# Performance work log

Hardware: AMD Instinct MI355X
Metric: run time of the kernel (lower is better)

The kernel has to match this reference:

```python
import jax, jax.numpy as jnp
import numpy as np
import math

B, N, C, S, H, E = 2, 20000, 512, 128, 8, 320000
D = C // H
EPS = 1e-6


def setup_inputs() -> dict:
    key = jax.random.key(0)
    ks = jax.random.split(key, 14)
    x = jax.random.normal(ks[0], (B, N, C), jnp.float32)
    adj_indices = jax.random.randint(ks[1], (2, E), 0, N)
    adj_values = jax.random.uniform(ks[2], (E,), jnp.float32)

    def lin(k, fi, fo):
        # stored as (in, out) so y = x @ W + b (equivalent to torch Linear)
        return jax.random.normal(k, (fi, fo), jnp.float32) / np.sqrt(fi).astype(np.float32)

    Ws = lin(ks[3], C, S); bs = jnp.zeros((S,), jnp.float32)
    Wq = lin(ks[4], C, C); bq = jnp.zeros((C,), jnp.float32)
    Wk = lin(ks[5], C, C); bk = jnp.zeros((C,), jnp.float32)
    Wv = lin(ks[6], C, C); bv = jnp.zeros((C,), jnp.float32)
    Wo = lin(ks[7], C, C); bo = jnp.zeros((C,), jnp.float32)
    beta_raw = jnp.float32(math.log(math.expm1(0.13)))
    return {"x": x, "adj_indices": adj_indices, "adj_values": adj_values,
            "Ws": Ws, "bs": bs, "Wq": Wq, "bq": bq, "Wk": Wk, "bk": bk,
            "Wv": Wv, "bv": bv, "Wo": Wo, "bo": bo, "beta_raw": beta_raw}


def reference(x, adj_indices, adj_values, Ws, bs, Wq, bq, Wk, bk, Wv, bv, Wo, bo, beta_raw):
    # slice assignment weights: (B, N, S)
    weights = jax.nn.softmax(x @ Ws + bs, axis=-1)
    # weight_sum -> (B, S, 1), clamped
    wsum = jnp.maximum(weights.sum(axis=1), EPS)[:, :, None]
    slices = jnp.einsum('bns,bnc->bsc', weights, x) / wsum  # (B, S, C)

    # sparse adjacency aggregation: y[b, r] = sum_e v_e * weights[b, col_e]
    rows, cols = adj_indices[0], adj_indices[1]
    msg = jnp.take(weights, cols, axis=1) * adj_values[None, :, None]  # (B, E, S)
    graph_weights = jax.vmap(lambda m: jax.ops.segment_sum(m, rows, num_segments=N))(msg)  # (B, N, S)

    gb = jnp.einsum('bns,bnt->bst', weights, graph_weights)  # (B, S, S)
    gb = 0.5 * (gb + jnp.swapaxes(gb, 1, 2))
    gb = gb / jnp.maximum(gb.sum(axis=-1, keepdims=True), EPS)
    gb = jnp.log(jnp.maximum(gb, EPS))

    def heads(t, W, b):
        return (t @ W + b).reshape(B, S, H, D).transpose(0, 2, 1, 3)  # (B, H, S, D)

    q = heads(slices, Wq, bq)
    k = heads(slices, Wk, bk)
    v = heads(slices, Wv, bv)
    logits = jnp.einsum('bhqd,bhkd->bhqk', q, k) / math.sqrt(D)
    logits = logits + jax.nn.softplus(beta_raw) * gb[:, None]
    attn = jax.nn.softmax(logits, axis=-1)
    slices_out = jnp.einsum('bhqk,bhkd->bhqd', attn, v).transpose(0, 2, 1, 3).reshape(B, S, C)
    slices_out = slices_out @ Wo + bo
    return jnp.einsum('bns,bsc->bnc', weights, slices_out)  # (B, N, C)
```

## Files before the change

kernel.cpp:

```cpp
#include <hip/hip_runtime.h>
#include <math.h>

#define Bn 2
#define Nn 20000
#define Cn 512
#define Sn 128
#define Hn 8
#define Dn 64
#define En 320000
#define EPSf 1e-6f
#define NB64 313
#define NB128 157

#define S_CHUNK 320
#define S_KB 63
#define G_CHUNK 128
#define G_KB 157

typedef __attribute__((ext_vector_type(4))) float f32x4;
typedef __attribute__((ext_vector_type(8))) short s16x8;

__device__ __forceinline__ unsigned short f2bf(float f) {
    unsigned u = __float_as_uint(f);
    return (unsigned short)((u + 0x7fffu + ((u >> 16) & 1u)) >> 16);
}
__device__ __forceinline__ float bf2f(unsigned short h) {
    return __uint_as_float(((unsigned)h) << 16);
}

__device__ __forceinline__ unsigned lds_off(int row, int n) {
    unsigned ch = ((((unsigned)n >> 3) ^ ((unsigned)row & 7u) ^ (((unsigned)row >> 3) & 7u)) & 7u);
    return (unsigned)row * 128u + ch * 16u + ((unsigned)n & 7u) * 2u;
}

__device__ __forceinline__ void stage_bf16tile(
    const unsigned short* __restrict__ src, int stride, int nvalid, unsigned* dst, int t)
{
    #pragma unroll
    for (int l = 0; l < 2; l++) {
        int task = t + l * 256;
        int row = task >> 2, seg = task & 3;
        s16x8 a = {0,0,0,0,0,0,0,0}, b = {0,0,0,0,0,0,0,0};
        if (row < nvalid) {
            a = *(const s16x8*)(src + (size_t)row * stride + seg * 16);
            b = *(const s16x8*)(src + (size_t)row * stride + seg * 16 + 8);
        }
        *(s16x8*)((char*)dst + lds_off(row, seg * 16)) = a;
        *(s16x8*)((char*)dst + lds_off(row, seg * 16 + 8)) = b;
    }
}

__device__ __forceinline__ void stage_pairtile(
    const unsigned short* __restrict__ src, int stride, int c0,
    int nbase, int nlimit, unsigned* dst, int t)
{
    int c = t & 15;
    int p0 = t >> 4;
    #pragma unroll
    for (int half = 0; half < 2; half++) {
        int pp = p0 + half * 16;
        int nl = 2 * pp;
        int ng = nbase + nl;
        s16x8 a0 = {0,0,0,0,0,0,0,0}, a1 = {0,0,0,0,0,0,0,0};
        if (ng < nlimit)     a0 = *(const s16x8*)(src + (size_t)ng * stride + c0 + 8 * c);
        if (ng + 1 < nlimit) a1 = *(const s16x8*)(src + (size_t)(ng + 1) * stride + c0 + 8 * c);
        #pragma unroll
        for (int i = 0; i < 8; i++) {
            unsigned val = ((unsigned)(unsigned short)a0[i]) |
                           (((unsigned)(unsigned short)a1[i]) << 16);
            dst[lds_off(8 * c + i, nl) >> 2] = val;
        }
    }
}

__device__ __forceinline__ void stage_tilesF(
    const unsigned short* __restrict__ wA, const float* __restrict__ Bsrc,
    int Bstride, int c0, int nbase, unsigned* At32, unsigned* Bt32, int t)
{
    int c = t & 15;
    int p0 = t >> 4;
    #pragma unroll
    for (int half = 0; half < 2; half++) {
        int pp = p0 + half * 16;
        int nl = 2 * pp;
        int ng = nbase + nl;
        s16x8 a0 = {0,0,0,0,0,0,0,0}, a1 = {0,0,0,0,0,0,0,0};
        if (ng < Nn)     a0 = *(const s16x8*)(wA + (size_t)ng * Sn + 8 * c);
        if (ng + 1 < Nn) a1 = *(const s16x8*)(wA + (size_t)(ng + 1) * Sn + 8 * c);
        #pragma unroll
        for (int i = 0; i < 8; i++) {
            unsigned val = ((unsigned)(unsigned short)a0[i]) |
                           (((unsigned)(unsigned short)a1[i]) << 16);
            At32[lds_off(8 * c + i, nl) >> 2] = val;
        }
        float b0[8], b1[8];
        if (ng < Nn) {
            float4 v0 = *(const float4*)(Bsrc + (size_t)ng * Bstride + c0 + 8 * c);
            float4 v1 = *(const float4*)(Bsrc + (size_t)ng * Bstride + c0 + 8 * c + 4);
            b0[0]=v0.x; b0[1]=v0.y; b0[2]=v0.z; b0[3]=v0.w;
            b0[4]=v1.x; b0[5]=v1.y; b0[6]=v1.z; b0[7]=v1.w;
        } else {
            #pragma unroll
            for (int i = 0; i < 8; i++) b0[i] = 0.f;
        }
        if (ng + 1 < Nn) {
            float4 v0 = *(const float4*)(Bsrc + (size_t)(ng + 1) * Bstride + c0 + 8 * c);
            float4 v1 = *(const float4*)(Bsrc + (size_t)(ng + 1) * Bstride + c0 + 8 * c + 4);
            b1[0]=v0.x; b1[1]=v0.y; b1[2]=v0.z; b1[3]=v0.w;
            b1[4]=v1.x; b1[5]=v1.y; b1[6]=v1.z; b1[7]=v1.w;
        } else {
            #pragma unroll
            for (int i = 0; i < 8; i++) b1[i] = 0.f;
        }
        #pragma unroll
        for (int i = 0; i < 8; i++) {
            unsigned val = (unsigned)f2bf(b0[i]) | (((unsigned)f2bf(b1[i])) << 16);
            Bt32[lds_off(8 * c + i, nl) >> 2] = val;
        }
    }
}

__global__ __launch_bounds__(256) void k_prepWsT(
    const float* __restrict__ Ws, unsigned short* __restrict__ WsT)
{
    __shared__ float tile[32][33];
    int t = threadIdx.x;
    int k0 = blockIdx.x * 32;
    int s0 = blockIdx.y * 32;
    #pragma unroll
    for (int l = 0; l < 4; l++) {
        int idx = t + l * 256;
        int r = idx >> 5, c = idx & 31;
        tile[r][c] = Ws[(size_t)(k0 + r) * Sn + s0 + c];
    }
    __syncthreads();
    #pragma unroll
    for (int l = 0; l < 4; l++) {
        int idx = t + l * 256;
        int r = idx >> 5, c = idx & 31;
        WsT[(size_t)(s0 + r) * Cn + k0 + c] = f2bf(tile[c][r]);
    }
}

__global__ __launch_bounds__(256) void k_prepWT(
    const float* __restrict__ Wq, const float* __restrict__ Wk,
    const float* __restrict__ Wv, const float* __restrict__ Wo,
    unsigned short* __restrict__ WT)
{
    __shared__ float tile[32][33];
    int t = threadIdx.x;
    int z = blockIdx.z;
    const float* W = (z == 0) ? Wq : (z == 1) ? Wk : (z == 2) ? Wv : Wo;
    unsigned short* dst = WT + (size_t)z * Cn * Cn;
    int k0 = blockIdx.x * 32;
    int c0 = blockIdx.y * 32;
    #pragma unroll
    for (int l = 0; l < 4; l++) {
        int idx = t + l * 256;
        int r = idx >> 5, c = idx & 31;
        tile[r][c] = W[(size_t)(k0 + r) * Cn + c0 + c];
    }
    __syncthreads();
    #pragma unroll
    for (int l = 0; l < 4; l++) {
        int idx = t + l * 256;
        int r = idx >> 5, c = idx & 31;
        dst[(size_t)(c0 + r) * Cn + k0 + c] = f2bf(tile[c][r]);
    }
}

__global__ __launch_bounds__(256) void k_assign2(
    const float* __restrict__ x, const unsigned short* __restrict__ WsT,
    const float* __restrict__ bs, unsigned short* __restrict__ weights,
    float* __restrict__ wsum)
{
    __shared__ __align__(16) unsigned At32[2048];
    __shared__ __align__(16) unsigned Bt32[4096];
    __shared__ float wsum_loc[128];

    int t = threadIdx.x;
    int lane = t & 63;
    int wid = t >> 6;
    int l15 = lane & 15, lg = lane >> 4;
    int blk = blockIdx.x;
    int b = blk / NB64;
    int rb = blk % NB64;
    int n0 = rb * 64;
    int nvalid = Nn - n0; if (nvalid > 64) nvalid = 64;
    const float* xb = x + (size_t)b * Nn * Cn;

    if (t < 128) wsum_loc[t] = 0.f;

    f32x4 acc[8];
    const f32x4 fz = {0.f, 0.f, 0.f, 0.f};
    #pragma unroll
    for (int j = 0; j < 8; j++) acc[j] = fz;

    for (int ks = 0; ks < 8; ks++) {
        {
            int row = t >> 2, seg = t & 3;
            float v[16];
            if (row < nvalid) {
                const float4* p = (const float4*)(xb + (size_t)(n0 + row) * Cn + ks * 64 + seg * 16);
                float4 a = p[0], bq = p[1], c = p[2], d = p[3];
                v[0]=a.x; v[1]=a.y; v[2]=a.z; v[3]=a.w;
                v[4]=bq.x; v[5]=bq.y; v[6]=bq.z; v[7]=bq.w;
                v[8]=c.x; v[9]=c.y; v[10]=c.z; v[11]=c.w;
                v[12]=d.x; v[13]=d.y; v[14]=d.z; v[15]=d.w;
            } else {
                #pragma unroll
                for (int i = 0; i < 16; i++) v[i] = 0.f;
            }
            #pragma unroll
            for (int h = 0; h < 2; h++) {
                uint4 u;
                u.x = (unsigned)f2bf(v[h*8+0]) | (((unsigned)f2bf(v[h*8+1])) << 16);
                u.y = (unsigned)f2bf(v[h*8+2]) | (((unsigned)f2bf(v[h*8+3])) << 16);
                u.z = (unsigned)f2bf(v[h*8+4]) | (((unsigned)f2bf(v[h*8+5])) << 16);
                u.w = (unsigned)f2bf(v[h*8+6]) | (((unsigned)f2bf(v[h*8+7])) << 16);
                *(uint4*)((char*)At32 + lds_off(row, seg * 16 + h * 8)) = u;
            }
        }
        stage_bf16tile(WsT + ks * 64, Cn, 128, Bt32, t);
        __syncthreads();
        #pragma unroll
        for (int m = 0; m < 2; m++) {
            s16x8 af = *(const s16x8*)((const char*)At32 +
                       lds_off(wid * 16 + l15, m * 32 + lg * 8));
            #pragma unroll
            for (int j = 0; j < 8; j++) {
                s16x8 bf = *(const s16x8*)((const char*)Bt32 +
                           lds_off(j * 16 + l15, m * 32 + lg * 8));
                acc[j] = __builtin_amdgcn_mfma_f32_16x16x32_bf16(af, bf, acc[j], 0, 0, 0);
            }
        }
        __syncthreads();
    }

    float bsv[8];
    #pragma unroll
    for (int j = 0; j < 8; j++) bsv[j] = bs[j * 16 + l15];

    unsigned short* wb = weights + (size_t)b * Nn * Sn;
    float wacc[8] = {0.f,0.f,0.f,0.f,0.f,0.f,0.f,0.f};
    #pragma unroll
    for (int r = 0; r < 4; r++) {
        float lv[8];
        #pragma unroll
        for (int j = 0; j < 8; j++) lv[j] = acc[j][r] + bsv[j];
        float m = lv[0];
        #pragma unroll
        for (int j = 1; j < 8; j++) m = fmaxf(m, lv[j]);
        m = fmaxf(m, __shfl_xor(m, 1));
        m = fmaxf(m, __shfl_xor(m, 2));
        m = fmaxf(m, __shfl_xor(m, 4));
        m = fmaxf(m, __shfl_xor(m, 8));
        float e[8], sm = 0.f;
        #pragma unroll
        for (int j = 0; j < 8; j++) { e[j] = __expf(lv[j] - m); sm += e[j]; }
        sm += __shfl_xor(sm, 1);
        sm += __shfl_xor(sm, 2);
        sm += __shfl_xor(sm, 4);
        sm += __shfl_xor(sm, 8);
        float inv = 1.f / sm;
        int n = n0 + wid * 16 + lg * 4 + r;
        bool valid = (n < Nn);
        #pragma unroll
        for (int j = 0; j < 8; j++) {
            float w = e[j] * inv;
            if (valid) {
                wb[(size_t)n * Sn + j * 16 + l15] = f2bf(w);
                wacc[j] += w;
            }
        }
    }
    #pragma unroll
    for (int j = 0; j < 8; j++) {
        wacc[j] += __shfl_xor(wacc[j], 16);
        wacc[j] += __shfl_xor(wacc[j], 32);
    }
    if (lg == 0) {
        #pragma unroll
        for (int j = 0; j < 8; j++) atomicAdd(&wsum_loc[j * 16 + l15], wacc[j]);
    }
    __syncthreads();
    if (t < 128) atomicAdd(&wsum[b * Sn + t], wsum_loc[t]);
}

__global__ __launch_bounds__(256) void k_deg(
    const int* __restrict__ adj, int* __restrict__ deg)
{
    int e = blockIdx.x * 256 + threadIdx.x;
    if (e < En) atomicAdd(&deg[adj[e]], 1);
}

__global__ __launch_bounds__(1024) void k_scan(
    const int* __restrict__ deg, int* __restrict__ offs)
{
    __shared__ int wsums[16];
    __shared__ int excl[16];
    __shared__ int runsS;
    __shared__ int totS;
    int t = threadIdx.x;
    int lane = t & 63;
    int w = t >> 6;
    if (t == 0) { offs[0] = 0; runsS = 0; }
    __syncthreads();
    for (int base = 0; base < Nn; base += 1024) {
        int v = (base + t < Nn) ? deg[base + t] : 0;
        int sv = v;
        #pragma unroll
        for (int d = 1; d < 64; d <<= 1) {
            int u = __shfl_up(sv, d);
            if (lane >= d) sv += u;
        }
        if (lane == 63) wsums[w] = sv;
        __syncthreads();
        if (t < 16) {
            int xv = wsums[t];
            int sw = xv;
            #pragma unroll
            for (int d = 1; d < 16; d <<= 1) {
                int u = __shfl_up(sw, d);
                if (t >= d) sw += u;
            }
            excl[t] = sw - xv;
            if (t == 15) totS = sw;
        }
        __syncthreads();
        if (base + t < Nn) offs[base + t + 1] = runsS + excl[w] + sv;
        __syncthreads();
        if (t == 0) runsS += totS;
        __syncthreads();
    }
}

__global__ __launch_bounds__(256) void k_fill(
    const int* __restrict__ adj, const float* __restrict__ vals,
    const int* __restrict__ offs, int* __restrict__ cursor,
    int2* __restrict__ epack)
{
    int e = blockIdx.x * 256 + threadIdx.x;
    if (e < En) {
        int r = adj[e];
        int p = atomicAdd(&cursor[r], 1);
        epack[offs[r] + p] = make_int2(adj[En + e], __float_as_int(vals[e]));
    }
}

__global__ __launch_bounds__(128) void k_gather(
    const unsigned short* __restrict__ weights, const int2* __restrict__ epack,
    const int* __restrict__ offs, unsigned short* __restrict__ gwb)
{
    int r = blockIdx.x;
    int s = threadIdx.x;
    int o0 = offs[r], o1 = offs[r + 1];
    const unsigned short* w0 = weights;
    const unsigned short* w1 = weights + (size_t)Nn * Sn;
    float a0 = 0.f, a1 = 0.f;
    int j = o0;
    for (; j + 4 <= o1; j += 4) {
        int2 e0 = epack[j], e1 = epack[j + 1], e2 = epack[j + 2], e3 = epack[j + 3];
        float v0 = __int_as_float(e0.y), v1 = __int_as_float(e1.y);
        float v2 = __int_as_float(e2.y), v3 = __int_as_float(e3.y);
        float p00 = bf2f(w0[(size_t)e0.x * Sn + s]);
        float p01 = bf2f(w1[(size_t)e0.x * Sn + s]);
        float p10 = bf2f(w0[(size_t)e1.x * Sn + s]);
        float p11 = bf2f(w1[(size_t)e1.x * Sn + s]);
        float p20 = bf2f(w0[(size_t)e2.x * Sn + s]);
        float p21 = bf2f(w1[(size_t)e2.x * Sn + s]);
        float p30 = bf2f(w0[(size_t)e3.x * Sn + s]);
        float p31 = bf2f(w1[(size_t)e3.x * Sn + s]);
        a0 += v0 * p00 + v1 * p10 + v2 * p20 + v3 * p30;
        a1 += v0 * p01 + v1 * p11 + v2 * p21 + v3 * p31;
    }
    for (; j < o1; j++) {
        int2 e = epack[j];
        float v = __int_as_float(e.y);
        a0 += v * bf2f(w0[(size_t)e.x * Sn + s]);
        a1 += v * bf2f(w1[(size_t)e.x * Sn + s]);
    }
    gwb[(size_t)r * Sn + s] = f2bf(a0);
    gwb[(size_t)Nn * Sn + (size_t)r * Sn + s] = f2bf(a1);
}

__global__ __launch_bounds__(256) void k_mmS(
    const unsigned short* __restrict__ wAall, const float* __restrict__ xall,
    float* __restrict__ partial)
{
    __shared__ __align__(16) unsigned At32[4096];
    __shared__ __align__(16) unsigned Bt32[4096];
    int t = threadIdx.x;
    int lane = t & 63;
    int wid = t >> 6;
    int ws = wid & 1, wc = wid >> 1;
    int blk = blockIdx.x;
    int b = blk / (4 * S_KB);
    int rem = blk % (4 * S_KB);
    int cb = rem / S_KB;
    int kb = rem % S_KB;
    int n0 = kb * S_CHUNK;
    int c0 = cb * 128;
    const unsigned short* wA = wAall + (size_t)b * Nn * Sn;
    const float* Bsrc = xall + (size_t)b * Nn * Cn;

    f32x4 acc[4][4];
    const f32x4 fz = {0.f, 0.f, 0.f, 0.f};
    #pragma unroll
    for (int i = 0; i < 4; i++) {
        #pragma unroll
        for (int j = 0; j < 4; j++) acc[i][j] = fz;
    }

    int l15 = lane & 15, lg = lane >> 4;

    for (int kt = 0; kt < S_CHUNK; kt += 64) {
        stage_tilesF(wA, Bsrc, Cn, c0, n0 + kt, At32, Bt32, t);
        __syncthreads();
        #pragma unroll
        for (int m = 0; m < 2; m++) {
            s16x8 af[4], bfr[4];
            #pragma unroll
            for (int i = 0; i < 4; i++) {
                int row = ws * 64 + i * 16 + l15;
                af[i] = *(const s16x8*)((const char*)At32 + lds_off(row, m * 32 + lg * 8));
            }
            #pragma unroll
            for (int j = 0; j < 4; j++) {
                int row = wc * 64 + j * 16 + l15;
                bfr[j] = *(const s16x8*)((const char*)Bt32 + lds_off(row, m * 32 + lg * 8));
            }
            #pragma unroll
            for (int i = 0; i < 4; i++) {
                #pragma unroll
                for (int j = 0; j < 4; j++)
                    acc[i][j] = __builtin_amdgcn_mfma_f32_16x16x32_bf16(
                        af[i], bfr[j], acc[i][j], 0, 0, 0);
            }
        }
        __syncthreads();
    }

    float* pp = partial + (size_t)blk * 16384;
    #pragma unroll
    for (int i = 0; i < 4; i++) {
        int srow = ws * 64 + i * 16 + lg * 4;
        #pragma unroll
        for (int j = 0; j < 4; j++) {
            int ccol = wc * 64 + j * 16 + l15;
            #pragma unroll
            for (int r = 0; r < 4; r++)
                pp[(size_t)(srow + r) * 128 + ccol] = acc[i][j][r];
        }
    }
}

__global__ __launch_bounds__(256) void k_mmG(
    const unsigned short* __restrict__ wAall, const unsigned short* __restrict__ gwall,
    float* __restrict__ partial)
{
    __shared__ __align__(16) unsigned At32[4096];
    __shared__ __align__(16) unsigned Bt32[4096];
    int t = threadIdx.x;
    int lane = t & 63;
    int wid = t >> 6;
    int ws = wid & 1, wc = wid >> 1;
    int blk = blockIdx.x;
    int b = blk / G_KB;
    int kb = blk % G_KB;
    int n0 = kb * G_CHUNK;
    const unsigned short* wA = wAall + (size_t)b * Nn * Sn;
    const unsigned short* Bsrc = gwall + (size_t)b * Nn * Sn;

    f32x4 acc[4][4];
    const f32x4 fz = {0.f, 0.f, 0.f, 0.f};
    #pragma unroll
    for (int i = 0; i < 4; i++) {
        #pragma unroll
        for (int j = 0; j < 4; j++) acc[i][j] = fz;
    }

    int l15 = lane & 15, lg = lane >> 4;

    for (int kt = 0; kt < G_CHUNK; kt += 64) {
        stage_pairtile(wA, Sn, 0, n0 + kt, Nn, At32, t);
        stage_pairtile(Bsrc, Sn, 0, n0 + kt, Nn, Bt32, t);
        __syncthreads();
        #pragma unroll
        for (int m = 0; m < 2; m++) {
            s16x8 af[4], bfr[4];
            #pragma unroll
            for (int i = 0; i < 4; i++) {
                int row = ws * 64 + i * 16 + l15;
                af[i] = *(const s16x8*)((const char*)At32 + lds_off(row, m * 32 + lg * 8));
            }
            #pragma unroll
            for (int j = 0; j < 4; j++) {
                int row = wc * 64 + j * 16 + l15;
                bfr[j] = *(const s16x8*)((const char*)Bt32 + lds_off(row, m * 32 + lg * 8));
            }
            #pragma unroll
            for (int i = 0; i < 4; i++) {
                #pragma unroll
                for (int j = 0; j < 4; j++)
                    acc[i][j] = __builtin_amdgcn_mfma_f32_16x16x32_bf16(
                        af[i], bfr[j], acc[i][j], 0, 0, 0);
            }
        }
        __syncthreads();
    }

    float* pp = partial + (size_t)blk * 16384;
    #pragma unroll
    for (int i = 0; i < 4; i++) {
        int srow = ws * 64 + i * 16 + lg * 4;
        #pragma unroll
        for (int j = 0; j < 4; j++) {
            int ccol = wc * 64 + j * 16 + l15;
            #pragma unroll
            for (int r = 0; r < 4; r++)
                pp[(size_t)(srow + r) * 128 + ccol] = acc[i][j][r];
        }
    }
}

__global__ __launch_bounds__(256) void k_reduceS(
    const float* __restrict__ partial, const float* __restrict__ wsum,
    unsigned short* __restrict__ sl16)
{
    int g = blockIdx.x * 256 + threadIdx.x;
    int c = g & 127;
    int s = (g >> 7) & 127;
    int cb = (g >> 14) & 3;
    int b = g >> 16;
    const float* pp = partial + (size_t)(b * 4 + cb) * S_KB * 16384 + (size_t)s * 128 + c;
    float sum = 0.f;
    #pragma unroll 7
    for (int kb = 0; kb < S_KB; kb++) sum += pp[(size_t)kb * 16384];
    sl16[((size_t)b * Sn + s) * Cn + cb * 128 + c] =
        f2bf(sum / fmaxf(wsum[b * Sn + s], EPSf));
}

__global__ __launch_bounds__(256) void k_reduceG(
    const float* __restrict__ partial, float* __restrict__ gb_raw)
{
    int g = blockIdx.x * 256 + threadIdx.x;
    int t2 = g & 127;
    int s = (g >> 7) & 127;
    int b = g >> 14;
    const float* pp = partial + (size_t)b * G_KB * 16384 + (size_t)s * 128 + t2;
    float sum = 0.f;
    #pragma unroll 8
    for (int kb = 0; kb < G_KB; kb++) sum += pp[(size_t)kb * 16384];
    gb_raw[(size_t)b * 16384 + (size_t)s * 128 + t2] = sum;
}

__global__ __launch_bounds__(128) void k_gb_fin(
    const float* __restrict__ gb_raw, float* __restrict__ gb)
{
    int bid = blockIdx.x;
    int b = bid >> 7, i = bid & 127;
    int j = threadIdx.x;
    const float* gr = gb_raw + (size_t)b * Sn * Sn;
    float sym = 0.5f * (gr[i * Sn + j] + gr[j * Sn + i]);
    float sum = sym;
    #pragma unroll
    for (int d = 1; d < 64; d <<= 1) sum += __shfl_xor(sum, d);
    __shared__ float wred[2];
    if ((j & 63) == 0) wred[j >> 6] = sum;
    __syncthreads();
    sum = wred[0] + wred[1];
    float r = fmaxf(sum, EPSf);
    gb[(size_t)b * Sn * Sn + (size_t)i * Sn + j] = logf(fmaxf(sym / r, EPSf));
}

__global__ __launch_bounds__(256) void k_qkv(
    const unsigned short* __restrict__ sl16, const unsigned short* __restrict__ WT,
    const float* __restrict__ bq, const float* __restrict__ bk,
    const float* __restrict__ bv,
    float* __restrict__ q, float* __restrict__ kb, float* __restrict__ vb)
{
    __shared__ __align__(16) unsigned At32[4096];
    __shared__ __align__(16) unsigned Bt32[4096];
    int t = threadIdx.x;
    int lane = t & 63;
    int wid = t >> 6;
    int ws = wid & 1, wc = wid >> 1;
    int l15 = lane & 15, lg = lane >> 4;
    int rb = blockIdx.x, cb = blockIdx.y, sel = blockIdx.z;
    const unsigned short* Bmat = WT + (size_t)sel * Cn * Cn;
    const float* bias = (sel == 0) ? bq : (sel == 1) ? bk : bv;
    float* outp = (sel == 0) ? q : (sel == 1) ? kb : vb;

    f32x4 acc[4][4];
    const f32x4 fz = {0.f, 0.f, 0.f, 0.f};
    #pragma unroll
    for (int i = 0; i < 4; i++) {
        #pragma unroll
        for (int j = 0; j < 4; j++) acc[i][j] = fz;
    }

    for (int ks = 0; ks < 8; ks++) {
        stage_bf16tile(sl16 + (size_t)rb * 128 * Cn + ks * 64, Cn, 128, At32, t);
        stage_bf16tile(Bmat + (size_t)cb * 128 * Cn + ks * 64, Cn, 128, Bt32, t);
        __syncthreads();
        #pragma unroll
        for (int m = 0; m < 2; m++) {
            s16x8 af[4], bfr[4];
            #pragma unroll
            for (int i = 0; i < 4; i++)
                af[i] = *(const s16x8*)((const char*)At32 +
                        lds_off(ws * 64 + i * 16 + l15, m * 32 + lg * 8));
            #pragma unroll
            for (int j = 0; j < 4; j++)
                bfr[j] = *(const s16x8*)((const char*)Bt32 +
                        lds_off(wc * 64 + j * 16 + l15, m * 32 + lg * 8));
            #pragma unroll
            for (int i = 0; i < 4; i++) {
                #pragma unroll
                for (int j = 0; j < 4; j++)
                    acc[i][j] = __builtin_amdgcn_mfma_f32_16x16x32_bf16(
                        af[i], bfr[j], acc[i][j], 0, 0, 0);
            }
        }
        __syncthreads();
    }

    float bvv[4];
    #pragma unroll
    for (int j = 0; j < 4; j++) bvv[j] = bias[cb * 128 + wc * 64 + j * 16 + l15];
    #pragma unroll
    for (int i = 0; i < 4; i++) {
        #pragma unroll
        for (int r = 0; r < 4; r++) {
            int m = rb * 128 + ws * 64 + i * 16 + lg * 4 + r;
            #pragma unroll
            for (int j = 0; j < 4; j++)
                outp[(size_t)m * Cn + cb * 128 + wc * 64 + j * 16 + l15] =
                    acc[i][j][r] + bvv[j];
        }
    }
}

__global__ __launch_bounds__(128) void k_attn(
    const float* __restrict__ q, const float* __restrict__ k,
    const float* __restrict__ v, const float* __restrict__ gb,
    const float* __restrict__ beta_raw, unsigned short* __restrict__ attn16)
{
    __shared__ float kv[128][65];
    __shared__ float qv[64];
    __shared__ float p[128];
    __shared__ float wred[2][2];

    int t = threadIdx.x;
    int bid = blockIdx.x;
    int b = bid / (Hn * Sn);
    int h = (bid / Sn) % Hn;
    int i = bid % Sn;
    size_t base = (size_t)b * Sn * Cn + (size_t)h * Dn;

    if (t < 64) qv[t] = q[base + (size_t)i * Cn + t];
    for (int l = 0; l < 64; l++) {
        int idx = t + l * 128;
        int j = idx >> 6, d = idx & 63;
        kv[j][d] = k[base + (size_t)j * Cn + d];
    }
    __syncthreads();

    float dot = 0.f;
    #pragma unroll
    for (int d = 0; d < 64; d++) dot += qv[d] * kv[t][d];

    float beta = log1pf(__expf(beta_raw[0]));
    float logit = dot * 0.125f + beta * gb[(size_t)b * Sn * Sn + (size_t)i * Sn + t];

    float m = logit;
    #pragma unroll
    for (int d = 1; d < 64; d <<= 1) m = fmaxf(m, __shfl_xor(m, d));
    if ((t & 63) == 0) wred[0][t >> 6] = m;
    __syncthreads();
    m = fmaxf(wred[0][0], wred[0][1]);
    float e = __expf(logit - m);
    float sm = e;
    #pragma unroll
    for (int d = 1; d < 64; d <<= 1) sm += __shfl_xor(sm, d);
    if ((t & 63) == 0) wred[1][t >> 6] = sm;
    __syncthreads();
    sm = wred[1][0] + wred[1][1];
    p[t] = e / sm;
    __syncthreads();

    for (int l = 0; l < 64; l++) {
        int idx = t + l * 128;
        int j = idx >> 6, d = idx & 63;
        kv[j][d] = v[base + (size_t)j * Cn + d];
    }
    __syncthreads();

    if (t < 64) {
        float o = 0.f;
        #pragma unroll 8
        for (int j = 0; j < 128; j++) o += p[j] * kv[j][t];
        attn16[base + (size_t)i * Cn + t] = f2bf(o);
    }
}

__global__ __launch_bounds__(256) void k_wo(
    const unsigned short* __restrict__ attn16, const unsigned short* __restrict__ WoT,
    const float* __restrict__ bo, unsigned short* __restrict__ SoT)
{
    __shared__ __align__(16) unsigned At32[4096];
    __shared__ __align__(16) unsigned Bt32[4096];
    int t = threadIdx.x;
    int lane = t & 63;
    int wid = t >> 6;
    int ws = wid & 1, wc = wid >> 1;
    int l15 = lane & 15, lg = lane >> 4;
    int b = blockIdx.x, cb = blockIdx.y;

    f32x4 acc[4][4];
    const f32x4 fz = {0.f, 0.f, 0.f, 0.f};
    #pragma unroll
    for (int i = 0; i < 4; i++) {
        #pragma unroll
        for (int j = 0; j < 4; j++) acc[i][j] = fz;
    }

    for (int ks = 0; ks < 8; ks++) {
        stage_bf16tile(attn16 + (size_t)b * 128 * Cn + ks * 64, Cn, 128, At32, t);
        stage_bf16tile(WoT + (size_t)cb * 128 * Cn + ks * 64, Cn, 128, Bt32, t);
        __syncthreads();
        #pragma unroll
        for (int m = 0; m < 2; m++) {
            s16x8 af[4], bfr[4];
            #pragma unroll
            for (int i = 0; i < 4; i++)
                af[i] = *(const s16x8*)((const char*)At32 +
                        lds_off(ws * 64 + i * 16 + l15, m * 32 + lg * 8));
            #pragma unroll
            for (int j = 0; j < 4; j++)
                bfr[j] = *(const s16x8*)((const char*)Bt32 +
                        lds_off(wc * 64 + j * 16 + l15, m * 32 + lg * 8));
            #pragma unroll
            for (int i = 0; i < 4; i++) {
                #pragma unroll
                for (int j = 0; j < 4; j++)
                    acc[i][j] = __builtin_amdgcn_mfma_f32_16x16x32_bf16(
                        af[i], bfr[j], acc[i][j], 0, 0, 0);
            }
        }
        __syncthreads();
    }

    float bvv[4];
    #pragma unroll
    for (int j = 0; j < 4; j++) bvv[j] = bo[cb * 128 + wc * 64 + j * 16 + l15];
    unsigned short* sb = SoT + (size_t)b * Cn * Sn;
    #pragma unroll
    for (int i = 0; i < 4; i++) {
        #pragma unroll
        for (int j = 0; j < 4; j++) {
            int c = cb * 128 + wc * 64 + j * 16 + l15;
            #pragma unroll
            for (int r = 0; r < 4; r++) {
                int s = ws * 64 + i * 16 + lg * 4 + r;
                sb[(size_t)c * Sn + s] = f2bf(acc[i][j][r] + bvv[j]);
            }
        }
    }
}

__global__ __launch_bounds__(256) void k_out2(
    const unsigned short* __restrict__ wAll, const unsigned short* __restrict__ SoT,
    float* __restrict__ out)
{
    __shared__ __align__(16) unsigned At32[4096];
    __shared__ __align__(16) unsigned Bt32[4096];
    int t = threadIdx.x;
    int lane = t & 63;
    int wid = t >> 6;
    int ws = wid & 1, wc = wid >> 1;
    int l15 = lane & 15, lg = lane >> 4;
    int blk = blockIdx.x;
    int b = blk / (NB128 * 4);
    int rem = blk % (NB128 * 4);
    int rb = rem >> 2;
    int cb = rem & 3;
    int n0 = rb * 128, c0 = cb * 128;
    int nvalid = Nn - n0; if (nvalid > 128) nvalid = 128;
    const unsigned short* wb = wAll + (size_t)b * Nn * Sn;
    const unsigned short* sb = SoT + (size_t)b * Cn * Sn;

    f32x4 acc[4][4];
    const f32x4 fz = {0.f, 0.f, 0.f, 0.f};
    #pragma unroll
    for (int i = 0; i < 4; i++) {
        #pragma unroll
        for (int j = 0; j < 4; j++) acc[i][j] = fz;
    }

    #pragma unroll
    for (int ksi = 0; ksi < 2; ksi++) {
        stage_bf16tile(wb + (size_t)n0 * Sn + ksi * 64, Sn, nvalid, At32, t);
        stage_bf16tile(sb + (size_t)c0 * Sn + ksi * 64, Sn, 128, Bt32, t);
        __syncthreads();
        #pragma unroll
        for (int m = 0; m < 2; m++) {
            s16x8 af[4], bfr[4];
            #pragma unroll
            for (int i = 0; i < 4; i++)
                af[i] = *(const s16x8*)((const char*)At32 +
                        lds_off(ws * 64 + i * 16 + l15, m * 32 + lg * 8));
            #pragma unroll
            for (int j = 0; j < 4; j++)
                bfr[j] = *(const s16x8*)((const char*)Bt32 +
                        lds_off(wc * 64 + j * 16 + l15, m * 32 + lg * 8));
            #pragma unroll
            for (int i = 0; i < 4; i++) {
                #pragma unroll
                for (int j = 0; j < 4; j++)
                    acc[i][j] = __builtin_amdgcn_mfma_f32_16x16x32_bf16(
                        af[i], bfr[j], acc[i][j], 0, 0, 0);
            }
        }
        __syncthreads();
    }

    #pragma unroll
    for (int i = 0; i < 4; i++) {
        #pragma unroll
        for (int r = 0; r < 4; r++) {
            int n = n0 + ws * 64 + i * 16 + lg * 4 + r;
            if (n < Nn) {
                #pragma unroll
                for (int j = 0; j < 4; j++)
                    out[((size_t)b * Nn + n) * Cn + c0 + wc * 64 + j * 16 + l15] =
                        acc[i][j][r];
            }
        }
    }
}

extern "C" void kernel_launch(void* const* d_in, const int* in_sizes, int n_in,
                              void* d_out, int out_size, void* d_ws, size_t ws_size,
                              hipStream_t stream)
{
    const float* x  = (const float*)d_in[0];
    const int* adj  = (const int*)d_in[1];
    const float* av = (const float*)d_in[2];
    const float* Ws = (const float*)d_in[3];
    const float* bs = (const float*)d_in[4];
    const float* Wq = (const float*)d_in[5];
    const float* bq = (const float*)d_in[6];
    const float* Wk = (const float*)d_in[7];
    const float* bk = (const float*)d_in[8];
    const float* Wv = (const float*)d_in[9];
    const float* bv = (const float*)d_in[10];
    const float* Wo = (const float*)d_in[11];
    const float* bo = (const float*)d_in[12];
    const float* br = (const float*)d_in[13];
    float* out = (float*)d_out;
    (void)in_sizes; (void)n_in; (void)out_size; (void)ws_size;

    char* ws = (char*)d_ws;
    size_t off = 0;
    unsigned short* wb16  = (unsigned short*)(ws + off); off += (size_t)Bn * Nn * Sn * 2;
    unsigned short* gwb16 = (unsigned short*)(ws + off); off += (size_t)Bn * Nn * Sn * 2;
    unsigned short* sl16  = (unsigned short*)(ws + off); off += (size_t)Bn * Sn * Cn * 2;
    float* wsum       = (float*)(ws + off); off += 1024;
    float* gb_raw     = (float*)(ws + off); off += (size_t)Bn * Sn * Sn * 4;
    float* gb         = (float*)(ws + off); off += (size_t)Bn * Sn * Sn * 4;
    float* q          = (float*)(ws + off); off += (size_t)Bn * Sn * Cn * 4;
    float* kbuf       = (float*)(ws + off); off += (size_t)Bn * Sn * Cn * 4;
    float* vbuf       = (float*)(ws + off); off += (size_t)Bn * Sn * Cn * 4;
    unsigned short* attn16 = (unsigned short*)(ws + off); off += (size_t)Bn * Sn * Cn * 2;
    unsigned short* WsT = (unsigned short*)(ws + off); off += (size_t)Sn * Cn * 2;
    unsigned short* WT  = (unsigned short*)(ws + off); off += (size_t)4 * Cn * Cn * 2;
    unsigned short* SoT = (unsigned short*)(ws + off); off += (size_t)Bn * Cn * Sn * 2;
    char* U = ws + off;
    int*  deg    = (int*)(U);
    int*  cursor = (int*)(U + 80128);
    int*  offs   = (int*)(U + 160256);
    int2* epack  = (int2*)(U + 240640);
    float* partialS = (float*)U;
    float* partialG = (float*)U;

    hipMemsetAsync(wsum, 0, 1024, stream);
    hipMemsetAsync(U, 0, 160256, stream);

    k_prepWsT<<<dim3(16, 4), 256, 0, stream>>>(Ws, WsT);
    k_prepWT<<<dim3(16, 16, 4), 256, 0, stream>>>(Wq, Wk, Wv, Wo, WT);
    k_assign2<<<Bn * NB64, 256, 0, stream>>>(x, WsT, bs, wb16, wsum);

    k_deg<<<(En + 255) / 256, 256, 0, stream>>>(adj, deg);
    k_scan<<<1, 1024, 0, stream>>>(deg, offs);
    k_fill<<<(En + 255) / 256, 256, 0, stream>>>(adj, av, offs, cursor, epack);
    k_gather<<<Nn, 128, 0, stream>>>(wb16, epack, offs, gwb16);

    k_mmS<<<Bn * 4 * S_KB, 256, 0, stream>>>(wb16, x, partialS);
    k_reduceS<<<(Bn * Sn * Cn) / 256, 256, 0, stream>>>(partialS, wsum, sl16);

    k_mmG<<<Bn * G_KB, 256, 0, stream>>>(wb16, gwb16, partialG);
    k_reduceG<<<(Bn * Sn * Sn) / 256, 256, 0, stream>>>(partialG, gb_raw);
    k_gb_fin<<<Bn * Sn, 128, 0, stream>>>(gb_raw, gb);

    k_qkv<<<dim3(2, 4, 3), 256, 0, stream>>>(sl16, WT, bq, bk, bv, q, kbuf, vbuf);
    k_attn<<<Bn * Hn * Sn, 128, 0, stream>>>(q, kbuf, vbuf, gb, br, attn16);
    k_wo<<<dim3(2, 4), 256, 0, stream>>>(attn16, WT + (size_t)3 * Cn * Cn, bo, SoT);

    k_out2<<<Bn * NB128 * 4, 256, 0, stream>>>(wb16, SoT, out);
}
```

Measured before the change: 256.2 us.

## Double-buffer LDS tiles with register prefetch in assign and slice GEMMs; merge weight prep

The assign and slice-matmul kernels now prefetch the next K-tile's global data into registers while the current tile is computed from a second LDS buffer. The goal is to hide global-load latency behind the MFMA loop. The assign kernel also stages its softmax output through LDS so it can write coalesced 16-byte rows, and the two weight-transpose kernels are merged into one launch. The cost is doubled shared memory and more registers per thread, which may reduce occupancy.

```diff
diff --git a/kernel.cpp b/kernel.cpp
--- a/kernel.cpp
+++ b/kernel.cpp
@@ -73,92 +73,32 @@
     }
 }
 
-__device__ __forceinline__ void stage_tilesF(
-    const unsigned short* __restrict__ wA, const float* __restrict__ Bsrc,
-    int Bstride, int c0, int nbase, unsigned* At32, unsigned* Bt32, int t)
-{
-    int c = t & 15;
-    int p0 = t >> 4;
-    #pragma unroll
-    for (int half = 0; half < 2; half++) {
-        int pp = p0 + half * 16;
-        int nl = 2 * pp;
-        int ng = nbase + nl;
-        s16x8 a0 = {0,0,0,0,0,0,0,0}, a1 = {0,0,0,0,0,0,0,0};
-        if (ng < Nn)     a0 = *(const s16x8*)(wA + (size_t)ng * Sn + 8 * c);
-        if (ng + 1 < Nn) a1 = *(const s16x8*)(wA + (size_t)(ng + 1) * Sn + 8 * c);
-        #pragma unroll
-        for (int i = 0; i < 8; i++) {
-            unsigned val = ((unsigned)(unsigned short)a0[i]) |
-                           (((unsigned)(unsigned short)a1[i]) << 16);
-            At32[lds_off(8 * c + i, nl) >> 2] = val;
-        }
-        float b0[8], b1[8];
-        if (ng < Nn) {
-            float4 v0 = *(const float4*)(Bsrc + (size_t)ng * Bstride + c0 + 8 * c);
-            float4 v1 = *(const float4*)(Bsrc + (size_t)ng * Bstride + c0 + 8 * c + 4);
-            b0[0]=v0.x; b0[1]=v0.y; b0[2]=v0.z; b0[3]=v0.w;
-            b0[4]=v1.x; b0[5]=v1.y; b0[6]=v1.z; b0[7]=v1.w;
-        } else {
-            #pragma unroll
-            for (int i = 0; i < 8; i++) b0[i] = 0.f;
-        }
-        if (ng + 1 < Nn) {
-            float4 v0 = *(const float4*)(Bsrc + (size_t)(ng + 1) * Bstride + c0 + 8 * c);
-            float4 v1 = *(const float4*)(Bsrc + (size_t)(ng + 1) * Bstride + c0 + 8 * c + 4);
-            b1[0]=v0.x; b1[1]=v0.y; b1[2]=v0.z; b1[3]=v0.w;
-            b1[4]=v1.x; b1[5]=v1.y; b1[6]=v1.z; b1[7]=v1.w;
-        } else {
-            #pragma unroll
-            for (int i = 0; i < 8; i++) b1[i] = 0.f;
-        }
-        #pragma unroll
-        for (int i = 0; i < 8; i++) {
-            unsigned val = (unsigned)f2bf(b0[i]) | (((unsigned)f2bf(b1[i])) << 16);
-            Bt32[lds_off(8 * c + i, nl) >> 2] = val;
-        }
-    }
-}
-
-__global__ __launch_bounds__(256) void k_prepWsT(
-    const float* __restrict__ Ws, unsigned short* __restrict__ WsT)
+__global__ __launch_bounds__(256) void k_prepW(
+    const float* __restrict__ Ws, const float* __restrict__ Wq,
+    const float* __restrict__ Wk, const float* __restrict__ Wv,
+    const float* __restrict__ Wo, unsigned short* __restrict__ WsT,
+    unsigned short* __restrict__ WT)
 {
     __shared__ float tile[32][33];
     int t = threadIdx.x;
+    int z = blockIdx.z;
     int k0 = blockIdx.x * 32;
-    int s0 = blockIdx.y * 32;
+    int c0 = blockIdx.y * 32;
+    const float* W;
+    unsigned short* dst;
+    int ncols;
+    if (z == 0) {
+        if (c0 >= Sn) return;
+        W = Ws; dst = WsT; ncols = Sn;
+    } else {
+        W = (z == 1) ? Wq : (z == 2) ? Wk : (z == 3) ? Wv : Wo;
+        dst = WT + (size_t)(z - 1) * Cn * Cn; ncols = Cn;
+    }
     #pragma unroll
     for (int l = 0; l < 4; l++) {
         int idx = t + l * 256;
         int r = idx >> 5, c = idx & 31;
-        tile[r][c] = Ws[(size_t)(k0 + r) * Sn + s0 + c];
-    }
-    __syncthreads();
-    #pragma unroll
-    for (int l = 0; l < 4; l++) {
-        int idx = t + l * 256;
-        int r = idx >> 5, c = idx & 31;
-        WsT[(size_t)(s0 + r) * Cn + k0 + c] = f2bf(tile[c][r]);
-    }
-}
-
-__global__ __launch_bounds__(256) void k_prepWT(
-    const float* __restrict__ Wq, const float* __restrict__ Wk,
-    const float* __restrict__ Wv, const float* __restrict__ Wo,
-    unsigned short* __restrict__ WT)
-{
-    __shared__ float tile[32][33];
-    int t = threadIdx.x;
-    int z = blockIdx.z;
-    const float* W = (z == 0) ? Wq : (z == 1) ? Wk : (z == 2) ? Wv : Wo;
-    unsigned short* dst = WT + (size_t)z * Cn * Cn;
-    int k0 = blockIdx.x * 32;
-    int c0 = blockIdx.y * 32;
-    #pragma unroll
-    for (int l = 0; l < 4; l++) {
-        int idx = t + l * 256;
-        int r = idx >> 5, c = idx & 31;
-        tile[r][c] = W[(size_t)(k0 + r) * Cn + c0 + c];
+        tile[r][c] = W[(size_t)(k0 + r) * ncols + c0 + c];
     }
     __syncthreads();
     #pragma unroll
@@ -174,8 +114,8 @@
     const float* __restrict__ bs, unsigned short* __restrict__ weights,
     float* __restrict__ wsum)
 {
-    __shared__ __align__(16) unsigned At32[2048];
-    __shared__ __align__(16) unsigned Bt32[4096];
+    __shared__ __align__(16) unsigned At32[2][2048];
+    __shared__ __align__(16) unsigned Bt32[2][4096];
     __shared__ float wsum_loc[128];
 
     int t = threadIdx.x;
@@ -191,26 +131,34 @@
 
     if (t < 128) wsum_loc[t] = 0.f;
 
+    int arow = t >> 2, aseg = t & 3;
+    bool aok = (arow < nvalid);
+    const float4* aptr = (const float4*)(xb + (size_t)(n0 + arow) * Cn) + aseg * 4;
+    int brow = t >> 2, bseg = t & 3;
+    const unsigned short* bp0 = WsT + (size_t)brow * Cn + bseg * 16;
+    const unsigned short* bp1 = WsT + (size_t)(brow + 64) * Cn + bseg * 16;
+
+    const f32x4 fz = {0.f, 0.f, 0.f, 0.f};
     f32x4 acc[8];
-    const f32x4 fz = {0.f, 0.f, 0.f, 0.f};
     #pragma unroll
     for (int j = 0; j < 8; j++) acc[j] = fz;
 
+    float4 ra[4];
+    #pragma unroll
+    for (int i = 0; i < 4; i++) ra[i] = make_float4(0.f, 0.f, 0.f, 0.f);
+    s16x8 rb0a, rb0b, rb1a, rb1b;
+
+    if (aok) { ra[0] = aptr[0]; ra[1] = aptr[1]; ra[2] = aptr[2]; ra[3] = aptr[3]; }
+    rb0a = *(const s16x8*)(bp0);     rb0b = *(const s16x8*)(bp0 + 8);
+    rb1a = *(const s16x8*)(bp1);     rb1b = *(const s16x8*)(bp1 + 8);
+
+    int cur = 0;
     for (int ks = 0; ks < 8; ks++) {
         {
-            int row = t >> 2, seg = t & 3;
-            float v[16];
-            if (row < nvalid) {
-                const float4* p = (const float4*)(xb + (size_t)(n0 + row) * Cn + ks * 64 + seg * 16);
-                float4 a = p[0], bq = p[1], c = p[2], d = p[3];
-                v[0]=a.x; v[1]=a.y; v[2]=a.z; v[3]=a.w;
-                v[4]=bq.x; v[5]=bq.y; v[6]=bq.z; v[7]=bq.w;
-                v[8]=c.x; v[9]=c.y; v[10]=c.z; v[11]=c.w;
-                v[12]=d.x; v[13]=d.y; v[14]=d.z; v[15]=d.w;
-            } else {
-                #pragma unroll
-                for (int i = 0; i < 16; i++) v[i] = 0.f;
-            }
+            float v[16] = {ra[0].x, ra[0].y, ra[0].z, ra[0].w,
+                           ra[1].x, ra[1].y, ra[1].z, ra[1].w,
+                           ra[2].x, ra[2].y, ra[2].z, ra[2].w,
+                           ra[3].x, ra[3].y, ra[3].z, ra[3].w};
             #pragma unroll
             for (int h = 0; h < 2; h++) {
                 uint4 u;
@@ -218,23 +166,36 @@
                 u.y = (unsigned)f2bf(v[h*8+2]) | (((unsigned)f2bf(v[h*8+3])) << 16);
                 u.z = (unsigned)f2bf(v[h*8+4]) | (((unsigned)f2bf(v[h*8+5])) << 16);
                 u.w = (unsigned)f2bf(v[h*8+6]) | (((unsigned)f2bf(v[h*8+7])) << 16);
-                *(uint4*)((char*)At32 + lds_off(row, seg * 16 + h * 8)) = u;
-            }
-        }
-        stage_bf16tile(WsT + ks * 64, Cn, 128, Bt32, t);
+                *(uint4*)((char*)At32[cur] + lds_off(arow, aseg * 16 + h * 8)) = u;
+            }
+            *(s16x8*)((char*)Bt32[cur] + lds_off(brow, bseg * 16)) = rb0a;
+            *(s16x8*)((char*)Bt32[cur] + lds_off(brow, bseg * 16 + 8)) = rb0b;
+            *(s16x8*)((char*)Bt32[cur] + lds_off(brow + 64, bseg * 16)) = rb1a;
+            *(s16x8*)((char*)Bt32[cur] + lds_off(brow + 64, bseg * 16 + 8)) = rb1b;
+        }
+        if (ks < 7) {
+            int kn = ks + 1;
+            if (aok) {
+                ra[0] = aptr[kn*16]; ra[1] = aptr[kn*16+1];
+                ra[2] = aptr[kn*16+2]; ra[3] = aptr[kn*16+3];
+            }
+            rb0a = *(const s16x8*)(bp0 + kn*64); rb0b = *(const s16x8*)(bp0 + kn*64 + 8);
+            rb1a = *(const s16x8*)(bp1 + kn*64); rb1b = *(const s16x8*)(bp1 + kn*64 + 8);
+        }
         __syncthreads();
         #pragma unroll
         for (int m = 0; m < 2; m++) {
-            s16x8 af = *(const s16x8*)((const char*)At32 +
+            s16x8 af = *(const s16x8*)((const char*)At32[cur] +
                        lds_off(wid * 16 + l15, m * 32 + lg * 8));
             #pragma unroll
             for (int j = 0; j < 8; j++) {
-                s16x8 bf = *(const s16x8*)((const char*)Bt32 +
+                s16x8 bf = *(const s16x8*)((const char*)Bt32[cur] +
                            lds_off(j * 16 + l15, m * 32 + lg * 8));
                 acc[j] = __builtin_amdgcn_mfma_f32_16x16x32_bf16(af, bf, acc[j], 0, 0, 0);
             }
         }
         __syncthreads();
+        cur ^= 1;
     }
 
     float bsv[8];
@@ -242,6 +203,7 @@
     for (int j = 0; j < 8; j++) bsv[j] = bs[j * 16 + l15];
 
     unsigned short* wb = weights + (size_t)b * Nn * Sn;
+    unsigned short* wt = (unsigned short*)&At32[0][0];
     float wacc[8] = {0.f,0.f,0.f,0.f,0.f,0.f,0.f,0.f};
     #pragma unroll
     for (int r = 0; r < 4; r++) {
@@ -263,15 +225,13 @@
         sm += __shfl_xor(sm, 4);
         sm += __shfl_xor(sm, 8);
         float inv = 1.f / sm;
-        int n = n0 + wid * 16 + lg * 4 + r;
-        bool valid = (n < Nn);
+        int rloc = wid * 16 + lg * 4 + r;
+        bool valid = (n0 + rloc < Nn);
         #pragma unroll
         for (int j = 0; j < 8; j++) {
             float w = e[j] * inv;
-            if (valid) {
-                wb[(size_t)n * Sn + j * 16 + l15] = f2bf(w);
-                wacc[j] += w;
-            }
+            wt[rloc * 128 + j * 16 + l15] = f2bf(w);
+            if (valid) wacc[j] += w;
         }
     }
     #pragma unroll
@@ -284,6 +244,14 @@
         for (int j = 0; j < 8; j++) atomicAdd(&wsum_loc[j * 16 + l15], wacc[j]);
     }
     __syncthreads();
+    {
+        int orow = t >> 2, oseg = t & 3;
+        if (orow < nvalid) {
+            uint4* dst = (uint4*)(wb + (size_t)(n0 + orow) * Sn + oseg * 32);
+            const uint4* src = (const uint4*)(wt + (size_t)orow * 128 + oseg * 32);
+            dst[0] = src[0]; dst[1] = src[1]; dst[2] = src[2]; dst[3] = src[3];
+        }
+    }
     if (t < 128) atomicAdd(&wsum[b * Sn + t], wsum_loc[t]);
 }
 
@@ -388,8 +356,8 @@
     const unsigned short* __restrict__ wAall, const float* __restrict__ xall,
     float* __restrict__ partial)
 {
-    __shared__ __align__(16) unsigned At32[4096];
-    __shared__ __align__(16) unsigned Bt32[4096];
+    __shared__ __align__(16) unsigned At32[2][4096];
+    __shared__ __align__(16) unsigned Bt32[2][4096];
     int t = threadIdx.x;
     int lane = t & 63;
     int wid = t >> 6;
@@ -413,9 +381,60 @@
     }
 
     int l15 = lane & 15, lg = lane >> 4;
-
-    for (int kt = 0; kt < S_CHUNK; kt += 64) {
-        stage_tilesF(wA, Bsrc, Cn, c0, n0 + kt, At32, Bt32, t);
+    int c = t & 15;
+    int p0 = t >> 4;
+
+    s16x8 pa[2][2];
+    float4 pb[2][4];
+    const s16x8 z8 = {0,0,0,0,0,0,0,0};
+
+    auto LOADS = [&](int kt) {
+        #pragma unroll
+        for (int h = 0; h < 2; h++) {
+            int nl = 2 * (p0 + h * 16);
+            int ng = n0 + kt + nl;
+            pa[h][0] = z8; pa[h][1] = z8;
+            pb[h][0] = make_float4(0.f,0.f,0.f,0.f); pb[h][1] = pb[h][0];
+            pb[h][2] = pb[h][0]; pb[h][3] = pb[h][0];
+            if (ng < Nn) {
+                pa[h][0] = *(const s16x8*)(wA + (size_t)ng * Sn + 8 * c);
+                pb[h][0] = *(const float4*)(Bsrc + (size_t)ng * Cn + c0 + 8 * c);
+                pb[h][1] = *(const float4*)(Bsrc + (size_t)ng * Cn + c0 + 8 * c + 4);
+            }
+            if (ng + 1 < Nn) {
+                pa[h][1] = *(const s16x8*)(wA + (size_t)(ng + 1) * Sn + 8 * c);
+                pb[h][2] = *(const float4*)(Bsrc + (size_t)(ng + 1) * Cn + c0 + 8 * c);
+                pb[h][3] = *(const float4*)(Bsrc + (size_t)(ng + 1) * Cn + c0 + 8 * c + 4);
+            }
+        }
+    };
+    auto STORE = [&](int buf) {
+        #pragma unroll
+        for (int h = 0; h < 2; h++) {
+            int nl = 2 * (p0 + h * 16);
+            #pragma unroll
+            for (int i = 0; i < 8; i++) {
+                unsigned val = ((unsigned)(unsigned short)pa[h][0][i]) |
+                               (((unsigned)(unsigned short)pa[h][1][i]) << 16);
+                At32[buf][lds_off(8 * c + i, nl) >> 2] = val;
+            }
+            float b0[8] = {pb[h][0].x, pb[h][0].y, pb[h][0].z, pb[h][0].w,
+                           pb[h][1].x, pb[h][1].y, pb[h][1].z, pb[h][1].w};
+            float b1[8] = {pb[h][2].x, pb[h][2].y, pb[h][2].z, pb[h][2].w,
+                           pb[h][3].x, pb[h][3].y, pb[h][3].z, pb[h][3].w};
+            #pragma unroll
+            for (int i = 0; i < 8; i++) {
+                unsigned val = (unsigned)f2bf(b0[i]) | (((unsigned)f2bf(b1[i])) << 16);
+                Bt32[buf][lds_off(8 * c + i, nl) >> 2] = val;
+            }
+        }
+    };
+
+    LOADS(0);
+    int cur = 0;
+    for (int it = 0; it < 5; it++) {
+        STORE(cur);
+        if (it < 4) LOADS((it + 1) * 64);
         __syncthreads();
         #pragma unroll
         for (int m = 0; m < 2; m++) {
@@ -423,12 +442,12 @@
             #pragma unroll
             for (int i = 0; i < 4; i++) {
                 int row = ws * 64 + i * 16 + l15;
-                af[i] = *(const s16x8*)((const char*)At32 + lds_off(row, m * 32 + lg * 8));
+                af[i] = *(const s16x8*)((const char*)At32[cur] + lds_off(row, m * 32 + lg * 8));
             }
             #pragma unroll
             for (int j = 0; j < 4; j++) {
                 int row = wc * 64 + j * 16 + l15;
-                bfr[j] = *(const s16x8*)((const char*)Bt32 + lds_off(row, m * 32 + lg * 8));
+                bfr[j] = *(const s16x8*)((const char*)Bt32[cur] + lds_off(row, m * 32 + lg * 8));
             }
             #pragma unroll
             for (int i = 0; i < 4; i++) {
@@ -439,6 +458,7 @@
             }
         }
         __syncthreads();
+        cur ^= 1;
     }
 
     float* pp = partial + (size_t)blk * 16384;
@@ -888,8 +908,7 @@
     hipMemsetAsync(wsum, 0, 1024, stream);
     hipMemsetAsync(U, 0, 160256, stream);
 
-    k_prepWsT<<<dim3(16, 4), 256, 0, stream>>>(Ws, WsT);
-    k_prepWT<<<dim3(16, 16, 4), 256, 0, stream>>>(Wq, Wk, Wv, Wo, WT);
+    k_prepW<<<dim3(16, 16, 5), 256, 0, stream>>>(Ws, Wq, Wk, Wv, Wo, WsT, WT);
     k_assign2<<<Bn * NB64, 256, 0, stream>>>(x, WsT, bs, wb16, wsum);
 
     k_deg<<<(En + 255) / 256, 256, 0, stream>>>(adj, deg);
```

Result: no change. 253.8 us (-1.0%).
